# Optimization experiments

Measured on AMD Instinct MI355X. Metric: run time of the kernel, lower is better.

The kernel has to match this reference:

```python
import jax, jax.numpy as jnp
import numpy as np

TABLE_SIZE = 1_000_000
NUM_HASH = 4
EMB_DIM = 128
SEED = 42
SUB_DIM = EMB_DIM // NUM_HASH  # 32


def _hash_ids(ids, seed):
    """Vectorized integer hash (xxhash stand-in): 32-bit xorshift-multiply mix.
    ids: int32 array; seed: uint32 scalar. Returns int32 indices in [0, TABLE_SIZE).
    """
    x = ids.astype(jnp.uint32) + seed
    x = x ^ (x >> 16)
    x = x * jnp.uint32(0x7FEB352D)
    x = x ^ (x >> 15)
    x = x * jnp.uint32(0x846CA68B)
    x = x ^ (x >> 16)
    return (x % jnp.uint32(TABLE_SIZE)).astype(jnp.int32)


def setup_inputs() -> dict:
    key = jax.random.key(0)
    k_ids, k_tab = jax.random.split(key)
    input_ids = jax.random.randint(k_ids, (4096, 200), 0, 1_000_000_000, dtype=jnp.int32)
    # stacked per-hash embedding tables: [H, table_size, sub_dim]
    tables = jax.random.normal(k_tab, (NUM_HASH, TABLE_SIZE, SUB_DIM), dtype=jnp.float32)
    return {"input_ids": input_ids, "tables": tables}


def reference(input_ids, tables):
    orig_shape = input_ids.shape
    flat_ids = input_ids.reshape(-1)                       # [N]
    seeds = jnp.uint32(SEED) + jnp.arange(NUM_HASH, dtype=jnp.uint32)  # [H]
    # hashed indices per table: [H, N]
    idx = jax.vmap(lambda s: _hash_ids(flat_ids, s))(seeds)
    # per-table gather: [H, N, sub_dim]
    emb = jax.vmap(lambda tab, i: tab[i])(tables, idx)
    # concat along feature dim -> [N, H*sub_dim] == [N, EMB_DIM]
    out = jnp.moveaxis(emb, 0, 1).reshape(flat_ids.shape[0], EMB_DIM)
    return out.reshape(orig_shape + (EMB_DIM,))
```

## Files before the change

kernel.cpp:

```cpp
#include <hip/hip_runtime.h>
#include <cstdint>


#define TABLE_SIZE 1000000u
#define SEED 42u

__device__ __forceinline__ uint32_t hash_id(uint32_t x) {
    x ^= x >> 16;
    x *= 0x7FEB352Du;
    x ^= x >> 15;
    x *= 0x846CA68Bu;
    x ^= x >> 16;
    return x % TABLE_SIZE;
}

__global__ void bloom_emb_kernel(const int* __restrict__ ids,
                                 const float4* __restrict__ tables,
                                 float4* __restrict__ out,
                                 int n) {
    int tid = blockIdx.x * blockDim.x + threadIdx.x;
    int gid  = tid >> 5;
    int lane = tid & 31;
    if (gid >= n) return;

    int h  = lane >> 3;
    int d4 = lane & 7;

    uint32_t x = (uint32_t)ids[gid] + SEED + (uint32_t)h;
    uint32_t idx = hash_id(x);

    const float4 v = tables[((size_t)h * TABLE_SIZE + idx) * 8 + (size_t)d4];
    out[(size_t)gid * 32 + (size_t)lane] = v;
}

extern "C" void kernel_launch(void* const* d_in, const int* in_sizes, int n_in,
                              void* d_out, int out_size, void* d_ws, size_t ws_size,
                              hipStream_t stream) {
    const int*   ids    = (const int*)d_in[0];
    const float* tables = (const float*)d_in[1];
    float*       out    = (float*)d_out;

    const int n = in_sizes[0];
    const long long total_threads = (long long)n * 32;
    const int block = 256;
    const int grid = (int)((total_threads + block - 1) / block);

    bloom_emb_kernel<<<grid, block, 0, stream>>>(
        ids, (const float4*)tables, (float4*)out, n);
}
```

Measured before the change: 756.3 us.

## Split gather per hash table with cache-warming streaming pass before each

Replaces the single fused gather with four per-table passes. Each pass first streams the whole 128 MB table with a warm kernel so it sits in the large last-level cache, then gathers from it with nontemporal output stores. The aim is to turn random DRAM row accesses into cache hits, at the cost of reading every table sequentially in full and launching eight kernels.

```diff
diff --git a/kernel.cpp b/kernel.cpp
--- a/kernel.cpp
+++ b/kernel.cpp
@@ -4,6 +4,8 @@
 
 #define TABLE_SIZE 1000000u
 #define SEED 42u
+
+typedef float vfloat4 __attribute__((ext_vector_type(4)));
 
 __device__ __forceinline__ uint32_t hash_id(uint32_t x) {
     x ^= x >> 16;
@@ -14,37 +16,49 @@
     return x % TABLE_SIZE;
 }
 
-__global__ void bloom_emb_kernel(const int* __restrict__ ids,
-                                 const float4* __restrict__ tables,
-                                 float4* __restrict__ out,
-                                 int n) {
-    int tid = blockIdx.x * blockDim.x + threadIdx.x;
-    int gid  = tid >> 5;
-    int lane = tid & 31;
+__global__ void __launch_bounds__(256) warm_kernel(const vfloat4* __restrict__ tab,
+                                                   int nvec) {
+    float acc = 0.0f;
+    const int stride = gridDim.x * blockDim.x;
+    for (int i = blockIdx.x * blockDim.x + threadIdx.x; i < nvec; i += stride) {
+        const vfloat4 v = tab[i];
+        acc += v.x + v.y + v.z + v.w;
+    }
+    asm volatile("" :: "v"(acc));
+}
+
+__global__ void __launch_bounds__(256) gather_kernel(const int* __restrict__ ids,
+                                                     const vfloat4* __restrict__ tab,
+                                                     vfloat4* __restrict__ out,
+                                                     int n, uint32_t seed_h, int h) {
+    const int tid = blockIdx.x * blockDim.x + threadIdx.x;
+    const int gid = tid >> 3;
     if (gid >= n) return;
+    const int d4 = tid & 7;
 
-    int h  = lane >> 3;
-    int d4 = lane & 7;
-
-    uint32_t x = (uint32_t)ids[gid] + SEED + (uint32_t)h;
-    uint32_t idx = hash_id(x);
-
-    const float4 v = tables[((size_t)h * TABLE_SIZE + idx) * 8 + (size_t)d4];
-    out[(size_t)gid * 32 + (size_t)lane] = v;
+    const uint32_t idx = hash_id((uint32_t)ids[gid] + seed_h);
+    const vfloat4 v = tab[(size_t)idx * 8 + (size_t)d4];
+    __builtin_nontemporal_store(v, &out[(size_t)gid * 32 + (size_t)(h * 8 + d4)]);
 }
 
 extern "C" void kernel_launch(void* const* d_in, const int* in_sizes, int n_in,
                               void* d_out, int out_size, void* d_ws, size_t ws_size,
                               hipStream_t stream) {
-    const int*   ids    = (const int*)d_in[0];
-    const float* tables = (const float*)d_in[1];
-    float*       out    = (float*)d_out;
+    const int*     ids    = (const int*)d_in[0];
+    const vfloat4* tables = (const vfloat4*)d_in[1];
+    vfloat4*       out    = (vfloat4*)d_out;
 
     const int n = in_sizes[0];
-    const long long total_threads = (long long)n * 32;
-    const int block = 256;
-    const int grid = (int)((total_threads + block - 1) / block);
+    const int nvec = (int)(TABLE_SIZE * 8u);
 
-    bloom_emb_kernel<<<grid, block, 0, stream>>>(
-        ids, (const float4*)tables, (float4*)out, n);
+    const long long gthreads = (long long)n * 8;
+    const int gblock = 256;
+    const int ggrid  = (int)((gthreads + gblock - 1) / gblock);
+
+    for (int h = 0; h < 4; ++h) {
+        const vfloat4* tab = tables + (size_t)h * TABLE_SIZE * 8;
+        warm_kernel<<<2048, 256, 0, stream>>>(tab, nvec);
+        gather_kernel<<<ggrid, gblock, 0, stream>>>(ids, tab, out, n,
+                                                    SEED + (uint32_t)h, h);
+    }
 }
```

New measurement: 826.0 us. +9.2%, slower.
